# Kernel tuning notes

Measured on AMD Instinct MI355X. Metric: run time of the kernel, lower is better.

The kernel has to match this reference:

```python
import jax, jax.numpy as jnp
import numpy as np

EPS = 1e-5
LEAK = 0.1
N_NODES = 100000
N_EDGES = 2000000
N_NF = 16
N_EF = 19
DIMS = [N_NF * 2 + N_EF, 64, 64, 32, 16, 8, 2]


def setup_inputs() -> dict:
    key = jax.random.key(0)
    ks = jax.random.split(key, 20)
    inp = {
        'x': jax.random.normal(ks[0], (N_NODES, N_NF), dtype=jnp.float32),
        'e': jax.random.normal(ks[1], (N_EDGES, N_EF), dtype=jnp.float32),
        'edge_index': jax.random.randint(ks[2], (2, N_EDGES), 0, N_NODES, dtype=jnp.int64),
        'xbatch': jnp.zeros((N_NODES,), dtype=jnp.int64),
        'bn_node_g': jnp.ones((N_NF,), jnp.float32),
        'bn_node_b': jnp.zeros((N_NF,), jnp.float32),
        'bn_edge_g': jnp.ones((N_EF,), jnp.float32),
        'bn_edge_b': jnp.zeros((N_EF,), jnp.float32),
    }
    # MLP weights: Lin(51,64), Lin(64,64), Lin(64,32), Lin(32,16), Lin(16,8), Lin(8,2)
    for i in range(6):
        fan_in, fan_out = DIMS[i], DIMS[i + 1]
        bound = 1.0 / np.sqrt(fan_in)
        inp[f'W{i+1}'] = jax.random.uniform(ks[4 + 2 * i], (fan_in, fan_out), jnp.float32, -bound, bound)
        inp[f'b{i+1}'] = jax.random.uniform(ks[5 + 2 * i], (fan_out,), jnp.float32, -bound, bound)
    return inp


def _batchnorm(v, g, b):
    # training-mode BatchNorm1d: biased batch statistics
    m = jnp.mean(v, axis=0)
    var = jnp.mean(jnp.square(v - m), axis=0)
    return (v - m) * (g / jnp.sqrt(var + EPS)) + b


def _lrelu(v):
    return jnp.where(v >= 0, v, LEAK * v)


def reference(x, e, edge_index, xbatch, bn_node_g, bn_node_b, bn_edge_g, bn_edge_b,
              W1, b1, W2, b2, W3, b3, W4, b4, W5, b5, W6, b6):
    e = _batchnorm(e, bn_edge_g, bn_edge_b)
    x = _batchnorm(x, bn_node_g, bn_node_b)
    src = x[edge_index[0]]  # [E, n_nf]
    dst = x[edge_index[1]]  # [E, n_nf]
    h = jnp.concatenate([src, dst, e], axis=1)  # [E, 2*n_nf + n_ef]
    h = _lrelu(h @ W1 + b1)
    h = _lrelu(h @ W2 + b2)
    h = _lrelu(h @ W3 + b3)
    h = _lrelu(h @ W4 + b4)
    h = _lrelu(h @ W5 + b5)
    edge_pred = h @ W6 + b6  # [E, 2]
    return edge_pred
```

## Files before the change

### kernel.cpp

```cpp
#include <hip/hip_runtime.h>

#define LEAK 0.1f
#define BN_EPS 1e-5f

constexpr int N_NODES = 100000;
constexpr int N_EDGES = 2000000;
constexpr int N_NF = 16;
constexpr int N_EF = 19;
constexpr int D0 = 2 * N_NF + N_EF;
constexpr int D1 = 64, D2 = 64, D3 = 32, D4 = 16, D5 = 8, D6 = 2;

constexpr int OFF_E_SUM = 0;
constexpr int OFF_E_SQ  = 32;
constexpr int OFF_X_SUM = 64;
constexpr int OFF_X_SQ  = 96;
constexpr int OFF_W1P   = 256;
constexpr int OFF_B1P   = OFF_W1P + D0 * D1;

typedef __attribute__((ext_vector_type(8))) short short8;
typedef __attribute__((ext_vector_type(4))) short short4v;
typedef __attribute__((ext_vector_type(4))) float f32x4;

static __device__ __forceinline__ short f2bf(float f) {
  unsigned u = __builtin_bit_cast(unsigned, f);
  unsigned r = (u + 0x7FFFu + ((u >> 16) & 1u)) >> 16;
  return (short)r;
}

constexpr int SROWS = 256;
__global__ __launch_bounds__(256) void e_stats_kernel(const float* __restrict__ v,
                                                      float* __restrict__ acc_sum,
                                                      float* __restrict__ acc_sq) {
  __shared__ float lbuf[SROWS * N_EF];
  const int t = threadIdx.x;
  float s = 0.f, qq = 0.f;
  const int col = t % N_EF;
  const int rep = t / N_EF;
  const int nchunks = (N_EDGES + SROWS - 1) / SROWS;
  for (int c = blockIdx.x; c < nchunks; c += gridDim.x) {
    const int nr = min(SROWS, N_EDGES - c * SROWS);
    const int nf4 = nr * N_EF / 4;
    const float4* src = (const float4*)(v + (size_t)c * SROWS * N_EF);
    for (int i = t; i < nf4; i += 256) ((float4*)lbuf)[i] = src[i];
    __syncthreads();
    if (rep < 13) {
      for (int r = rep; r < nr; r += 13) {
        float x = lbuf[r * N_EF + col];
        s += x; qq += x * x;
      }
    }
    __syncthreads();
  }
  lbuf[t] = s; lbuf[256 + t] = qq;
  __syncthreads();
  if (t < N_EF) {
    float ts = 0.f, tq = 0.f;
#pragma unroll
    for (int rp = 0; rp < 13; rp++) {
      ts += lbuf[t + N_EF * rp];
      tq += lbuf[256 + t + N_EF * rp];
    }
    atomicAdd(&acc_sum[t], ts);
    atomicAdd(&acc_sq[t], tq);
  }
}

template <int NF>
__global__ void col_stats_kernel(const float* __restrict__ v, int nrows,
                                 float* __restrict__ acc_sum,
                                 float* __restrict__ acc_sq) {
  float s[NF], qq[NF];
#pragma unroll
  for (int k = 0; k < NF; k++) { s[k] = 0.f; qq[k] = 0.f; }
  int tid = blockIdx.x * blockDim.x + threadIdx.x;
  int stride = gridDim.x * blockDim.x;
  for (int r = tid; r < nrows; r += stride) {
    const float* __restrict__ row = v + (size_t)r * NF;
#pragma unroll
    for (int k = 0; k < NF; k++) { float t = row[k]; s[k] += t; qq[k] += t * t; }
  }
#pragma unroll
  for (int k = 0; k < NF; k++) {
#pragma unroll
    for (int off = 32; off > 0; off >>= 1) {
      s[k] += __shfl_down(s[k], off);
      qq[k] += __shfl_down(qq[k], off);
    }
  }
  __shared__ float ls[4][2 * NF];
  int wave = threadIdx.x >> 6;
  int lane = threadIdx.x & 63;
  if (lane == 0) {
#pragma unroll
    for (int k = 0; k < NF; k++) { ls[wave][k] = s[k]; ls[wave][NF + k] = qq[k]; }
  }
  __syncthreads();
  if (threadIdx.x < 2 * NF) {
    float t = ls[0][threadIdx.x] + ls[1][threadIdx.x] + ls[2][threadIdx.x] +
              ls[3][threadIdx.x];
    if (threadIdx.x < NF) atomicAdd(&acc_sum[threadIdx.x], t);
    else                  atomicAdd(&acc_sq[threadIdx.x - NF], t);
  }
}

__global__ void fold_bn_kernel(const float* __restrict__ ws,
                               const float* __restrict__ ng, const float* __restrict__ nb,
                               const float* __restrict__ eg, const float* __restrict__ eb,
                               const float* __restrict__ W1, const float* __restrict__ b1,
                               float* __restrict__ W1p, float* __restrict__ b1p) {
  __shared__ float sc[D0], sh[D0];
  int t = threadIdx.x;
  if (t < D0) {
    float mean, var, g, b;
    if (t < 2 * N_NF) {
      int k = t & (N_NF - 1);
      mean = ws[OFF_X_SUM + k] / (float)N_NODES;
      var  = ws[OFF_X_SQ + k] / (float)N_NODES - mean * mean;
      g = ng[k]; b = nb[k];
    } else {
      int k = t - 2 * N_NF;
      mean = ws[OFF_E_SUM + k] / (float)N_EDGES;
      var  = ws[OFF_E_SQ + k] / (float)N_EDGES - mean * mean;
      g = eg[k]; b = eb[k];
    }
    float scale = g / sqrtf(var + BN_EPS);
    sc[t] = scale;
    sh[t] = b - mean * scale;
  }
  __syncthreads();
  if (t < D1) {
    float accb = b1[t];
    for (int i = 0; i < D0; i++) {
      float w = W1[i * D1 + t];
      W1p[i * D1 + t] = w * sc[i];
      accb += sh[i] * w;
    }
    b1p[t] = accb;
  }
}


__device__ __forceinline__ short8 load_wfrag(const float* __restrict__ W, int ldn,
                                             int kbase, int nbase, int kmax, int nmax,
                                             int q, int g) {
  short8 f;
#pragma unroll
  for (int j = 0; j < 8; j++) {
    int k = kbase + g * 8 + j;
    int n = nbase + q;
    float w = (k < kmax && n < nmax) ? W[k * ldn + n] : 0.f;
    f[j] = f2bf(w);
  }
  return f;
}

struct Pref {
  float4 vs, vd;
  float e0, e1, e2, e3;
  float t0, t1, t2;
};

__device__ __forceinline__ Pref load_gather(int eidx, int g,
                                            const float* __restrict__ x,
                                            const float* __restrict__ e,
                                            const int* __restrict__ ei) {
  Pref p;
  const int src = ei[eidx];
  const int dst = ei[N_EDGES + eidx];
  p.vs = ((const float4*)x)[(size_t)src * 4 + g];
  p.vd = ((const float4*)x)[(size_t)dst * 4 + g];
  const float* er = e + (size_t)eidx * N_EF;
  p.e0 = er[g * 4 + 0]; p.e1 = er[g * 4 + 1];
  p.e2 = er[g * 4 + 2]; p.e3 = er[g * 4 + 3];
  if (g == 0) { p.t0 = er[16]; p.t1 = er[17]; p.t2 = er[18]; }
  else        { p.t0 = 0.f; p.t1 = 0.f; p.t2 = 0.f; }
  return p;
}

__device__ __forceinline__ void stage_row(char* lb, int row, int swzq, int g,
                                          const Pref& p) {
  char* base = lb + row * 128;
  short4v ps = {f2bf(p.vs.x), f2bf(p.vs.y), f2bf(p.vs.z), f2bf(p.vs.w)};
  *(short4v*)(base + ((g * 8) ^ swzq)) = ps;
  short4v pd = {f2bf(p.vd.x), f2bf(p.vd.y), f2bf(p.vd.z), f2bf(p.vd.w)};
  *(short4v*)(base + ((32 + g * 8) ^ swzq)) = pd;
  short4v pe = {f2bf(p.e0), f2bf(p.e1), f2bf(p.e2), f2bf(p.e3)};
  *(short4v*)(base + ((64 + g * 8) ^ swzq)) = pe;
  short4v pt = {f2bf(p.t0), f2bf(p.t1), f2bf(p.t2), 0};
  *(short4v*)(base + ((96 + g * 8) ^ swzq)) = pt;
}

template <int KT, int NT>
__device__ __forceinline__ void mfma_layer2(char* lb, int q, int g, int swzq,
                                            const short8 (&wf)[KT][NT],
                                            const float (&bv)[NT]) {
  short8 a0[KT], a1[KT];
#pragma unroll
  for (int kk = 0; kk < KT; kk++) {
    a0[kk] = *(const short8*)(lb + q * 128 + ((kk * 64 + g * 16) ^ swzq));
    a1[kk] = *(const short8*)(lb + (q + 16) * 128 + ((kk * 64 + g * 16) ^ swzq));
  }
  f32x4 acc0[NT], acc1[NT];
#pragma unroll
  for (int nt = 0; nt < NT; nt++) {
    acc0[nt] = (f32x4){bv[nt], bv[nt], bv[nt], bv[nt]};
    acc1[nt] = acc0[nt];
#pragma unroll
    for (int kk = 0; kk < KT; kk++) {
      acc0[nt] = __builtin_amdgcn_mfma_f32_16x16x32_bf16(a0[kk], wf[kk][nt], acc0[nt], 0, 0, 0);
      acc1[nt] = __builtin_amdgcn_mfma_f32_16x16x32_bf16(a1[kk], wf[kk][nt], acc1[nt], 0, 0, 0);
    }
  }
#pragma unroll
  for (int nt = 0; nt < NT; nt++) {
#pragma unroll
    for (int r = 0; r < 4; r++) {
      float v0 = acc0[nt][r];
      v0 = fmaxf(v0, LEAK * v0);
      int mw0 = 4 * g + r;
      *(short*)(lb + mw0 * 128 + ((nt * 32 + q * 2) ^ ((mw0 & 7) << 4))) = f2bf(v0);
      float v1 = acc1[nt][r];
      v1 = fmaxf(v1, LEAK * v1);
      int mw1 = 16 + 4 * g + r;
      *(short*)(lb + mw1 * 128 + ((nt * 32 + q * 2) ^ ((mw1 & 7) << 4))) = f2bf(v1);
    }
  }
}

#define RED16(v)                 \
  v += __shfl_xor(v, 1);         \
  v += __shfl_xor(v, 2);         \
  v += __shfl_xor(v, 4);         \
  v += __shfl_xor(v, 8);

__device__ __forceinline__ void tail56(char* lb, int roff, int q, int g, int swzq,
                                       short8 w5f, float b5v, float w60, float w61,
                                       float b60, float b61, float* out, int Eb) {
  short8 a5 = *(const short8*)(lb + (q + roff) * 128 + ((g * 16) ^ swzq));
  f32x4 acc5 = (f32x4){b5v, b5v, b5v, b5v};
  acc5 = __builtin_amdgcn_mfma_f32_16x16x32_bf16(a5, w5f, acc5, 0, 0, 0);
  float a50 = fmaxf(acc5[0], LEAK * acc5[0]);
  float a51 = fmaxf(acc5[1], LEAK * acc5[1]);
  float a52 = fmaxf(acc5[2], LEAK * acc5[2]);
  float a53 = fmaxf(acc5[3], LEAK * acc5[3]);
  float s00 = a50 * w60, s10 = a50 * w61;
  float s01 = a51 * w60, s11 = a51 * w61;
  float s02 = a52 * w60, s12 = a52 * w61;
  float s03 = a53 * w60, s13 = a53 * w61;
  RED16(s00) RED16(s10) RED16(s01) RED16(s11)
  RED16(s02) RED16(s12) RED16(s03) RED16(s13)
  if (q < 4) {
    float o0 = (q == 0) ? s00 : (q == 1) ? s01 : (q == 2) ? s02 : s03;
    float o1 = (q == 0) ? s10 : (q == 1) ? s11 : (q == 2) ? s12 : s13;
    ((float2*)out)[(size_t)Eb + roff + g * 4 + q] = make_float2(o0 + b60, o1 + b61);
  }
}

__global__ __launch_bounds__(256, 2) void edge_mlp_mfma_kernel(
    const float* __restrict__ x, const float* __restrict__ e,
    const int* __restrict__ ei,
    const float* __restrict__ W1p, const float* __restrict__ b1p,
    const float* __restrict__ W2, const float* __restrict__ b2,
    const float* __restrict__ W3, const float* __restrict__ b3,
    const float* __restrict__ W4, const float* __restrict__ b4,
    const float* __restrict__ W5, const float* __restrict__ b5,
    const float* __restrict__ W6, const float* __restrict__ b6,
    float* __restrict__ out) {
  __shared__ __align__(16) char actbuf[4 * 2 * 32 * 128];

  const int lane = threadIdx.x & 63;
  const int wave = threadIdx.x >> 6;
  const int q = lane & 15;
  const int g = lane >> 4;
  const int swzq = (q & 7) << 4;

  short8 w1f[2][4], w2f[2][4], w3f[2][2], w4f[1][1];
  float b1v[4], b2v[4], b3v[2], b4v[1];
#pragma unroll
  for (int kk = 0; kk < 2; kk++)
#pragma unroll
    for (int nt = 0; nt < 4; nt++) {
      w1f[kk][nt] = load_wfrag(W1p, 64, kk * 32, nt * 16, D0, 64, q, g);
      w2f[kk][nt] = load_wfrag(W2, 64, kk * 32, nt * 16, 64, 64, q, g);
    }
#pragma unroll
  for (int kk = 0; kk < 2; kk++)
#pragma unroll
    for (int nt = 0; nt < 2; nt++)
      w3f[kk][nt] = load_wfrag(W3, 32, kk * 32, nt * 16, 64, 32, q, g);
  w4f[0][0] = load_wfrag(W4, 16, 0, 0, 32, 16, q, g);
  short8 w5f = load_wfrag(W5, 8, 0, 0, 16, 8, q, g);
#pragma unroll
  for (int nt = 0; nt < 4; nt++) { b1v[nt] = b1p[nt * 16 + q]; b2v[nt] = b2[nt * 16 + q]; }
#pragma unroll
  for (int nt = 0; nt < 2; nt++) b3v[nt] = b3[nt * 16 + q];
  b4v[0] = b4[q];
  float b5v = (q < 8) ? b5[q] : 0.f;
  float w60 = (q < 8) ? W6[q * 2 + 0] : 0.f;
  float w61 = (q < 8) ? W6[q * 2 + 1] : 0.f;
  float b60 = b6[0], b61 = b6[1];

  const int n_bt = N_EDGES / 128;
  int buf = 0;
  int bt0 = blockIdx.x;
  Pref c1, c2;
  if (bt0 < n_bt) {
    const int Eb0 = bt0 * 128 + wave * 32;
    c1 = load_gather(Eb0 + q, g, x, e, ei);
    c2 = load_gather(Eb0 + 16 + q, g, x, e, ei);
  }
  for (int bt = bt0; bt < n_bt; bt += gridDim.x) {
    const int Eb = bt * 128 + wave * 32;
    const int nbt = bt + gridDim.x;
    Pref n1 = c1, n2 = c2;
    if (nbt < n_bt) {
      const int nEb = nbt * 128 + wave * 32;
      n1 = load_gather(nEb + q, g, x, e, ei);
      n2 = load_gather(nEb + 16 + q, g, x, e, ei);
    }
    char* lb = actbuf + wave * 8192 + buf * 4096;
    stage_row(lb, q, swzq, g, c1);
    stage_row(lb, q + 16, swzq, g, c2);
    mfma_layer2<2, 4>(lb, q, g, swzq, w1f, b1v);
    mfma_layer2<2, 4>(lb, q, g, swzq, w2f, b2v);
    mfma_layer2<2, 2>(lb, q, g, swzq, w3f, b3v);
    mfma_layer2<1, 1>(lb, q, g, swzq, w4f, b4v);
    tail56(lb, 0,  q, g, swzq, w5f, b5v, w60, w61, b60, b61, out, Eb);
    tail56(lb, 16, q, g, swzq, w5f, b5v, w60, w61, b60, b61, out, Eb);
    c1 = n1; c2 = n2; buf ^= 1;
  }
}

extern "C" void kernel_launch(void* const* d_in, const int* in_sizes, int n_in,
                              void* d_out, int out_size, void* d_ws, size_t ws_size,
                              hipStream_t stream) {
  const float* x  = (const float*)d_in[0];
  const float* e  = (const float*)d_in[1];
  const int*   ei = (const int*)d_in[2];
  const float* ng = (const float*)d_in[4];
  const float* nb = (const float*)d_in[5];
  const float* eg = (const float*)d_in[6];
  const float* eb = (const float*)d_in[7];
  const float* W1 = (const float*)d_in[8];
  const float* b1 = (const float*)d_in[9];
  const float* W2 = (const float*)d_in[10];
  const float* b2 = (const float*)d_in[11];
  const float* W3 = (const float*)d_in[12];
  const float* b3 = (const float*)d_in[13];
  const float* W4 = (const float*)d_in[14];
  const float* b4 = (const float*)d_in[15];
  const float* W5 = (const float*)d_in[16];
  const float* b5 = (const float*)d_in[17];
  const float* W6 = (const float*)d_in[18];
  const float* b6 = (const float*)d_in[19];
  float* out = (float*)d_out;
  float* ws  = (float*)d_ws;

  (void)hipMemsetAsync(ws, 0, 128 * sizeof(float), stream);

  e_stats_kernel<<<1024, 256, 0, stream>>>(e, ws + OFF_E_SUM, ws + OFF_E_SQ);
  col_stats_kernel<N_NF><<<128, 256, 0, stream>>>(x, N_NODES, ws + OFF_X_SUM, ws + OFF_X_SQ);
  fold_bn_kernel<<<1, 64, 0, stream>>>(ws, ng, nb, eg, eb, W1, b1,
                                       ws + OFF_W1P, ws + OFF_B1P);

  edge_mlp_mfma_kernel<<<2048, 256, 0, stream>>>(
      x, e, ei, ws + OFF_W1P, ws + OFF_B1P,
      W2, b2, W3, b3, W4, b4, W5, b5, W6, b6, out);
}
```

Baseline: 531.4 us.

## Restructure gather prefetch to load indices ahead and node rows in-loop

The software pipeline now prefetches only edge indices and edge features for the next tile. The dependent node-feature gathers are issued at the start of the current iteration, so fewer values stay live across the loop. The LDS activation buffer drops from double to single buffering, the occupancy hint is removed from launch bounds, and the grid is halved to 1024 blocks. The aim is lower register and LDS pressure, in exchange for exposing the x-gather latency inside each iteration with no cross-iteration prefetch for it.

```diff
diff --git a/kernel.cpp b/kernel.cpp
--- a/kernel.cpp
+++ b/kernel.cpp
@@ -154,39 +154,24 @@
   return f;
 }
 
-struct Pref {
-  float4 vs, vd;
-  float e0, e1, e2, e3;
-  float t0, t1, t2;
-};
-
-__device__ __forceinline__ Pref load_gather(int eidx, int g,
-                                            const float* __restrict__ x,
-                                            const float* __restrict__ e,
-                                            const int* __restrict__ ei) {
-  Pref p;
-  const int src = ei[eidx];
-  const int dst = ei[N_EDGES + eidx];
-  p.vs = ((const float4*)x)[(size_t)src * 4 + g];
-  p.vd = ((const float4*)x)[(size_t)dst * 4 + g];
-  const float* er = e + (size_t)eidx * N_EF;
-  p.e0 = er[g * 4 + 0]; p.e1 = er[g * 4 + 1];
-  p.e2 = er[g * 4 + 2]; p.e3 = er[g * 4 + 3];
-  if (g == 0) { p.t0 = er[16]; p.t1 = er[17]; p.t2 = er[18]; }
-  else        { p.t0 = 0.f; p.t1 = 0.f; p.t2 = 0.f; }
-  return p;
-}
-
-__device__ __forceinline__ void stage_row(char* lb, int row, int swzq, int g,
-                                          const Pref& p) {
+__device__ __forceinline__ void load_e7(const float* __restrict__ er, int g,
+                                        float (&o)[7]) {
+  o[0] = er[g * 4 + 0]; o[1] = er[g * 4 + 1];
+  o[2] = er[g * 4 + 2]; o[3] = er[g * 4 + 3];
+  if (g == 0) { o[4] = er[16]; o[5] = er[17]; o[6] = er[18]; }
+  else        { o[4] = 0.f; o[5] = 0.f; o[6] = 0.f; }
+}
+
+__device__ __forceinline__ void stage_row2(char* lb, int row, int swzq, int g,
+                                           float4 vs, float4 vd, const float (&ev)[7]) {
   char* base = lb + row * 128;
-  short4v ps = {f2bf(p.vs.x), f2bf(p.vs.y), f2bf(p.vs.z), f2bf(p.vs.w)};
+  short4v ps = {f2bf(vs.x), f2bf(vs.y), f2bf(vs.z), f2bf(vs.w)};
   *(short4v*)(base + ((g * 8) ^ swzq)) = ps;
-  short4v pd = {f2bf(p.vd.x), f2bf(p.vd.y), f2bf(p.vd.z), f2bf(p.vd.w)};
+  short4v pd = {f2bf(vd.x), f2bf(vd.y), f2bf(vd.z), f2bf(vd.w)};
   *(short4v*)(base + ((32 + g * 8) ^ swzq)) = pd;
-  short4v pe = {f2bf(p.e0), f2bf(p.e1), f2bf(p.e2), f2bf(p.e3)};
+  short4v pe = {f2bf(ev[0]), f2bf(ev[1]), f2bf(ev[2]), f2bf(ev[3])};
   *(short4v*)(base + ((64 + g * 8) ^ swzq)) = pe;
-  short4v pt = {f2bf(p.t0), f2bf(p.t1), f2bf(p.t2), 0};
+  short4v pt = {f2bf(ev[4]), f2bf(ev[5]), f2bf(ev[6]), 0};
   *(short4v*)(base + ((96 + g * 8) ^ swzq)) = pt;
 }
 
@@ -256,7 +241,7 @@
   }
 }
 
-__global__ __launch_bounds__(256, 2) void edge_mlp_mfma_kernel(
+__global__ __launch_bounds__(256) void edge_mlp_mfma_kernel(
     const float* __restrict__ x, const float* __restrict__ e,
     const int* __restrict__ ei,
     const float* __restrict__ W1p, const float* __restrict__ b1p,
@@ -266,13 +251,14 @@
     const float* __restrict__ W5, const float* __restrict__ b5,
     const float* __restrict__ W6, const float* __restrict__ b6,
     float* __restrict__ out) {
-  __shared__ __align__(16) char actbuf[4 * 2 * 32 * 128];
+  __shared__ __align__(16) char actbuf[4 * 32 * 128];
 
   const int lane = threadIdx.x & 63;
   const int wave = threadIdx.x >> 6;
   const int q = lane & 15;
   const int g = lane >> 4;
   const int swzq = (q & 7) << 4;
+  char* lb = actbuf + wave * 4096;
 
   short8 w1f[2][4], w2f[2][4], w3f[2][2], w4f[1][1];
   float b1v[4], b2v[4], b3v[2], b4v[1];
@@ -301,33 +287,45 @@
   float b60 = b6[0], b61 = b6[1];
 
   const int n_bt = N_EDGES / 128;
-  int buf = 0;
-  int bt0 = blockIdx.x;
-  Pref c1, c2;
-  if (bt0 < n_bt) {
-    const int Eb0 = bt0 * 128 + wave * 32;
-    c1 = load_gather(Eb0 + q, g, x, e, ei);
-    c2 = load_gather(Eb0 + 16 + q, g, x, e, ei);
-  }
-  for (int bt = bt0; bt < n_bt; bt += gridDim.x) {
+  int bt = blockIdx.x;
+  int s1 = 0, d1 = 0, s2 = 0, d2 = 0;
+  float e1[7] = {0, 0, 0, 0, 0, 0, 0}, e2[7] = {0, 0, 0, 0, 0, 0, 0};
+  if (bt < n_bt) {
+    const int Eb0 = bt * 128 + wave * 32;
+    s1 = ei[Eb0 + q];      d1 = ei[N_EDGES + Eb0 + q];
+    s2 = ei[Eb0 + 16 + q]; d2 = ei[N_EDGES + Eb0 + 16 + q];
+    load_e7(e + (size_t)(Eb0 + q) * N_EF, g, e1);
+    load_e7(e + (size_t)(Eb0 + 16 + q) * N_EF, g, e2);
+  }
+  for (; bt < n_bt; bt += gridDim.x) {
     const int Eb = bt * 128 + wave * 32;
+    float4 vs1 = ((const float4*)x)[(size_t)s1 * 4 + g];
+    float4 vd1 = ((const float4*)x)[(size_t)d1 * 4 + g];
+    float4 vs2 = ((const float4*)x)[(size_t)s2 * 4 + g];
+    float4 vd2 = ((const float4*)x)[(size_t)d2 * 4 + g];
     const int nbt = bt + gridDim.x;
-    Pref n1 = c1, n2 = c2;
+    int ns1 = s1, nd1 = d1, ns2 = s2, nd2 = d2;
+    float f1[7], f2[7];
+#pragma unroll
+    for (int i = 0; i < 7; i++) { f1[i] = e1[i]; f2[i] = e2[i]; }
     if (nbt < n_bt) {
       const int nEb = nbt * 128 + wave * 32;
-      n1 = load_gather(nEb + q, g, x, e, ei);
-      n2 = load_gather(nEb + 16 + q, g, x, e, ei);
-    }
-    char* lb = actbuf + wave * 8192 + buf * 4096;
-    stage_row(lb, q, swzq, g, c1);
-    stage_row(lb, q + 16, swzq, g, c2);
+      ns1 = ei[nEb + q];      nd1 = ei[N_EDGES + nEb + q];
+      ns2 = ei[nEb + 16 + q]; nd2 = ei[N_EDGES + nEb + 16 + q];
+      load_e7(e + (size_t)(nEb + q) * N_EF, g, f1);
+      load_e7(e + (size_t)(nEb + 16 + q) * N_EF, g, f2);
+    }
+    stage_row2(lb, q, swzq, g, vs1, vd1, e1);
+    stage_row2(lb, q + 16, swzq, g, vs2, vd2, e2);
     mfma_layer2<2, 4>(lb, q, g, swzq, w1f, b1v);
     mfma_layer2<2, 4>(lb, q, g, swzq, w2f, b2v);
     mfma_layer2<2, 2>(lb, q, g, swzq, w3f, b3v);
     mfma_layer2<1, 1>(lb, q, g, swzq, w4f, b4v);
     tail56(lb, 0,  q, g, swzq, w5f, b5v, w60, w61, b60, b61, out, Eb);
     tail56(lb, 16, q, g, swzq, w5f, b5v, w60, w61, b60, b61, out, Eb);
-    c1 = n1; c2 = n2; buf ^= 1;
+    s1 = ns1; d1 = nd1; s2 = ns2; d2 = nd2;
+#pragma unroll
+    for (int i = 0; i < 7; i++) { e1[i] = f1[i]; e2[i] = f2[i]; }
   }
 }
 
@@ -363,7 +361,7 @@
   fold_bn_kernel<<<1, 64, 0, stream>>>(ws, ng, nb, eg, eb, W1, b1,
                                        ws + OFF_W1P, ws + OFF_B1P);
 
-  edge_mlp_mfma_kernel<<<2048, 256, 0, stream>>>(
+  edge_mlp_mfma_kernel<<<1024, 256, 0, stream>>>(
       x, e, ei, ws + OFF_W1P, ws + OFF_B1P,
       W2, b2, W3, b3, W4, b4, W5, b5, W6, b6, out);
 }
```

After: 537.7 us. No clear change (+1.2%).
